# Kernel tuning notes

Hardware: AMD Instinct MI355X
Metric: run time of the kernel (lower is better)

Reference implementation:

```python
import jax, jax.numpy as jnp
import numpy as np

N_R, N_C = 20000, 5000
E_R, E_C = 320000, 80000
D_IN, HID, OUT, K = 6, 128, 3, 3
NEG_SLOPE = 0.2


def gat_layer(x, edge_index, W, a_src, a_dst, b):
    """PyG GATConv (heads=1, concat=True, add_self_loops=True), eval mode."""
    n = x.shape[0]
    loop = jnp.arange(n, dtype=edge_index.dtype)
    src = jnp.concatenate([edge_index[0], loop])
    dst = jnp.concatenate([edge_index[1], loop])
    h = x @ W                                   # [n, HID]
    e_src = h @ a_src                           # [n]
    e_dst = h @ a_dst
    e = jax.nn.leaky_relu(e_src[src] + e_dst[dst], NEG_SLOPE)  # [E+n]
    m = jax.ops.segment_max(e, dst, num_segments=n)
    m = jnp.where(jnp.isfinite(m), m, 0.0)
    ex = jnp.exp(e - m[dst])
    denom = jax.ops.segment_sum(ex, dst, num_segments=n)
    alpha = ex / jnp.maximum(denom[dst], 1e-16)
    return jax.ops.segment_sum(alpha[:, None] * h[src], dst, num_segments=n) + b


def setup_inputs() -> dict:
    key = jax.random.key(0)
    ks = jax.random.split(key, 32)
    inp = {
        "x_resting": jax.random.normal(ks[0], (N_R, D_IN), jnp.float32),
        "x_collider": jax.random.normal(ks[1], (N_C, D_IN), jnp.float32),
        "edge_index_resting": jax.random.randint(ks[2], (2, E_R), 0, N_R, jnp.int32),
        "edge_index_collider": jax.random.randint(ks[3], (2, E_C), 0, N_C, jnp.int32),
        "knn_k": K,
    }
    i = 4
    for g in ("r", "c"):
        d_in = D_IN
        for l in (1, 2):
            inp[f"W_{g}{l}"] = jax.random.normal(ks[i], (d_in, HID), jnp.float32) * (1.0 / np.sqrt(d_in)); i += 1
            inp[f"as_{g}{l}"] = jax.random.normal(ks[i], (HID,), jnp.float32) * 0.1; i += 1
            inp[f"ad_{g}{l}"] = jax.random.normal(ks[i], (HID,), jnp.float32) * 0.1; i += 1
            inp[f"b_{g}{l}"] = jnp.zeros((HID,), jnp.float32); i += 1
            d_in = HID
    inp["W_dec"] = jax.random.normal(ks[i], (2 * HID, OUT), jnp.float32) * (1.0 / np.sqrt(2 * HID)); i += 1
    inp["b_dec"] = jnp.zeros((OUT,), jnp.float32)
    return inp


def reference(x_resting, x_collider, edge_index_resting, edge_index_collider, knn_k,
              W_r1, as_r1, ad_r1, b_r1, W_r2, as_r2, ad_r2, b_r2,
              W_c1, as_c1, ad_c1, b_c1, W_c2, as_c2, ad_c2, b_c2,
              W_dec, b_dec):
    # resting branch (dropout is identity in eval mode)
    h_r = jax.nn.relu(gat_layer(x_resting, edge_index_resting, W_r1, as_r1, ad_r1, b_r1))
    h_r = jax.nn.relu(gat_layer(h_r, edge_index_resting, W_r2, as_r2, ad_r2, b_r2))
    # collider branch
    h_c = jax.nn.relu(gat_layer(x_collider, edge_index_collider, W_c1, as_c1, ad_c1, b_c1))
    h_c = jax.nn.relu(gat_layer(h_c, edge_index_collider, W_c2, as_c2, ad_c2, b_c2))
    # brute-force KNN: for each collider node, k nearest resting nodes (in feature space)
    d2 = (jnp.sum(h_c * h_c, 1)[:, None] + jnp.sum(h_r * h_r, 1)[None, :]
          - 2.0 * h_c @ h_r.T)                       # [N_C, N_R]
    _, nn_idx = jax.lax.top_k(-d2, knn_k)            # [N_C, k] indices into resting
    n_r = h_r.shape[0]
    flat_idx = nn_idx.reshape(-1)
    rep_c = jnp.repeat(h_c, knn_k, axis=0)           # x_collider[col]
    pooled_sum = jax.ops.segment_sum(rep_c, flat_idx, num_segments=n_r)
    cnt = jax.ops.segment_sum(jnp.ones((flat_idx.shape[0],), h_c.dtype), flat_idx, num_segments=n_r)
    pooled = pooled_sum / jnp.maximum(cnt, 1.0)[:, None]  # scatter_mean (0 for empty)
    x_combined = jnp.concatenate([h_r, pooled], axis=-1)
    return x_combined @ W_dec + b_dec                # new positions [N_R, 3]
```

## Files before the change

### kernel.cpp

```cpp
#include <hip/hip_runtime.h>
#include <hip/hip_bf16.h>

#define HID 128
#define NEG_SLOPE 0.2f
#define CSPLIT 8
#define KNN_CB 64
#define NCAND (CSPLIT * 12)

typedef _Float16 f16x8 __attribute__((ext_vector_type(8)));
typedef float f32x4 __attribute__((ext_vector_type(4)));

__device__ __forceinline__ bool cand_lt(float d1, int i1, float d2, int i2) {
    return d1 < d2 || (d1 == d2 && i1 < i2);
}
__device__ __forceinline__ void ins3(float s, int r, float fd[3], int fi[3]) {
    if (!cand_lt(s, r, fd[2], fi[2])) return;
    if (cand_lt(s, r, fd[0], fi[0])) {
        fd[2]=fd[1];fi[2]=fi[1]; fd[1]=fd[0];fi[1]=fi[0]; fd[0]=s;fi[0]=r;
    } else if (cand_lt(s, r, fd[1], fi[1])) {
        fd[2]=fd[1];fi[2]=fi[1]; fd[1]=s;fi[1]=r;
    } else {
        fd[2]=s;fi[2]=r;
    }
}

__global__ void k_deg(const int* __restrict__ ei, int E, int n, int* __restrict__ deg) {
    int i = blockIdx.x * blockDim.x + threadIdx.x;
    if (i >= E + n) return;
    int d = (i < E) ? ei[E + i] : i - E;
    atomicAdd(&deg[d], 1);
}

__global__ void k_chunksum(const int* __restrict__ deg, int* __restrict__ bsum, int n) {
    int t = threadIdx.x;
    int i = blockIdx.x * 256 + t;
    int v = (i < n) ? deg[i] : 0;
#pragma unroll
    for (int o = 1; o < 64; o <<= 1) v += __shfl_xor(v, o);
    __shared__ int wsum[4];
    if ((t & 63) == 0) wsum[t >> 6] = v;
    __syncthreads();
    if (t == 0) bsum[blockIdx.x] = wsum[0] + wsum[1] + wsum[2] + wsum[3];
}

__global__ void k_scan_small(int* __restrict__ a, int nb) {
    __shared__ int buf[256];
    int t = threadIdx.x;
    int v = (t < nb) ? a[t] : 0;
    buf[t] = v;
    __syncthreads();
    for (int o = 1; o < 256; o <<= 1) {
        int add = (t >= o) ? buf[t - o] : 0;
        __syncthreads();
        buf[t] += add;
        __syncthreads();
    }
    if (t < nb) a[t] = buf[t] - v;
    if (t == 0) a[nb] = buf[nb - 1];
}

__global__ void k_scan_apply(const int* __restrict__ deg, const int* __restrict__ bsum,
                             int* __restrict__ off, int* __restrict__ cur, int n) {
    __shared__ int buf[256];
    int b = blockIdx.x, t = threadIdx.x;
    int i = b * 256 + t;
    int v = (i < n) ? deg[i] : 0;
    buf[t] = v;
    __syncthreads();
    for (int o = 1; o < 256; o <<= 1) {
        int add = (t >= o) ? buf[t - o] : 0;
        __syncthreads();
        buf[t] += add;
        __syncthreads();
    }
    int excl = bsum[b] + buf[t] - v;
    if (i < n) { off[i] = excl; cur[i] = excl; }
    if (b == 0 && t == 0) off[n] = bsum[gridDim.x];
}

__global__ void k_scatter(const int* __restrict__ ei, int E, int n,
                          int* __restrict__ cursor, int* __restrict__ csr) {
    int i = blockIdx.x * blockDim.x + threadIdx.x;
    if (i >= E + n) return;
    int s, d;
    if (i < E) { s = ei[i]; d = ei[E + i]; } else { s = d = i - E; }
    int pos = atomicAdd(&cursor[d], 1);
    csr[pos] = s;
}

__global__ __launch_bounds__(128) void k_linear(
    const float* __restrict__ x, const float* __restrict__ W,
    const float* __restrict__ a_src, const float* __restrict__ a_dst,
    float* __restrict__ h, float* __restrict__ es, float* __restrict__ ed,
    int d_in, int n) {
    int n0 = blockIdx.x * 4;
    int t = threadIdx.x;
    int w = t >> 6, lane = t & 63;
    __shared__ float xs[4][HID];
    __shared__ float p1[2], p2[2];
#pragma unroll
    for (int u = 0; u < 4; ++u) {
        int node = n0 + u;
        if (t < d_in) xs[u][t] = (node < n) ? x[(size_t)node * d_in + t] : 0.f;
    }
    __syncthreads();
    float acc[4] = {0.f, 0.f, 0.f, 0.f};
    for (int k = 0; k < d_in; ++k) {
        float wv = W[k * HID + t];
#pragma unroll
        for (int u = 0; u < 4; ++u) acc[u] += xs[u][k] * wv;
    }
    float asv = a_src[t], adv = a_dst[t];
    for (int u = 0; u < 4; ++u) {
        int node = n0 + u;
        if (node >= n) break;
        h[(size_t)node * HID + t] = acc[u];
        float v1 = acc[u] * asv, v2 = acc[u] * adv;
#pragma unroll
        for (int o = 32; o > 0; o >>= 1) { v1 += __shfl_xor(v1, o); v2 += __shfl_xor(v2, o); }
        if (lane == 0) { p1[w] = v1; p2[w] = v2; }
        __syncthreads();
        if (t == 0) { es[node] = p1[0] + p1[1]; ed[node] = p2[0] + p2[1]; }
        __syncthreads();
    }
}

__global__ __launch_bounds__(256) void k_gat_csr(
    const int* __restrict__ off, const int* __restrict__ csr,
    const float* __restrict__ es, const float* __restrict__ ed,
    const float* __restrict__ h, const float* __restrict__ b,
    float* __restrict__ agg, int n,
    _Float16* __restrict__ h16, float* __restrict__ n2) {
    int node = blockIdx.x * 4 + (threadIdx.x >> 6);
    int lane = threadIdx.x & 63;
    if (node >= n) return;
    int beg = off[node], end = off[node + 1];
    float edd = ed[node];
    float m = -INFINITY;
    for (int j = beg + lane; j < end; j += 64) {
        int s = csr[j];
        float e = es[s] + edd;
        e = e > 0.f ? e : NEG_SLOPE * e;
        m = fmaxf(m, e);
    }
#pragma unroll
    for (int o = 32; o > 0; o >>= 1) m = fmaxf(m, __shfl_xor(m, o));
    float den = 0.f, a0 = 0.f, a1 = 0.f;
    int j = beg;
    for (; j + 1 < end; j += 2) {
        int s0 = csr[j], s1 = csr[j + 1];
        float e0 = es[s0] + edd;
        float e1 = es[s1] + edd;
        e0 = e0 > 0.f ? e0 : NEG_SLOPE * e0;
        e1 = e1 > 0.f ? e1 : NEG_SLOPE * e1;
        float ex0 = expf(e0 - m);
        float ex1 = expf(e1 - m);
        float h00 = h[(size_t)s0 * HID + lane];
        float h01 = h[(size_t)s0 * HID + 64 + lane];
        float h10 = h[(size_t)s1 * HID + lane];
        float h11 = h[(size_t)s1 * HID + 64 + lane];
        den += ex0 + ex1;
        a0 += ex0 * h00 + ex1 * h10;
        a1 += ex0 * h01 + ex1 * h11;
    }
    if (j < end) {
        int s0 = csr[j];
        float e0 = es[s0] + edd;
        e0 = e0 > 0.f ? e0 : NEG_SLOPE * e0;
        float ex0 = expf(e0 - m);
        den += ex0;
        a0 += ex0 * h[(size_t)s0 * HID + lane];
        a1 += ex0 * h[(size_t)s0 * HID + 64 + lane];
    }
    float inv = 1.f / fmaxf(den, 1e-16f);
    float v0 = a0 * inv + b[lane];
    float v1 = a1 * inv + b[64 + lane];
    float r0 = v0 > 0.f ? v0 : 0.f;
    float r1 = v1 > 0.f ? v1 : 0.f;
    agg[(size_t)node * HID + lane] = r0;
    agg[(size_t)node * HID + 64 + lane] = r1;
    if (h16) {
        h16[(size_t)node * HID + lane] = (_Float16)r0;
        h16[(size_t)node * HID + 64 + lane] = (_Float16)r1;
    }
    if (n2) {
        float s2 = r0 * r0 + r1 * r1;
#pragma unroll
        for (int o = 32; o > 0; o >>= 1) s2 += __shfl_xor(s2, o);
        if (lane == 0) n2[node] = s2;
    }
}

__global__ __launch_bounds__(256) void k_knn_scan(
    const _Float16* __restrict__ hr2, const _Float16* __restrict__ hc2,
    const float* __restrict__ nr2, int n_c, int n_r, int rs_chunk,
    int* __restrict__ cand_i) {
    __shared__ _Float16 lds[2][64 * HID];
    int t = threadIdx.x, w = t >> 6, lane = t & 63;
    int li = lane & 15, q = lane >> 4;
    int c0 = blockIdx.x * KNN_CB;
    int split = blockIdx.y;
    int rbeg = split * rs_chunk;
    int rows = min(rs_chunk, n_r - rbeg);
    int rend = rbeg + rows;

    if (rows <= 0) {
        int c = c0 + w * 16 + li;
        if (c < n_c) {
            size_t base = ((size_t)(c * CSPLIT + split) * 4 + q) * 3;
            for (int k = 0; k < 3; ++k) cand_i[base + k] = 0x7fffffff;
        }
        return;
    }

    f16x8 bf[4];
    {
        int c = c0 + w * 16 + li;
        int cc = min(c, n_c - 1);
#pragma unroll
        for (int ks = 0; ks < 4; ++ks)
            bf[ks] = *(const f16x8*)(hc2 + (size_t)cc * HID + ks * 32 + q * 8);
    }

    float bd[3]; int bi[3];
#pragma unroll
    for (int k = 0; k < 3; ++k) { bd[k] = INFINITY; bi[k] = 0x7fffffff; }

    int nch = (rows + 63) >> 6;

    auto STAGE = [&](int bsel, int R) {
#pragma unroll
        for (int j = 0; j < 4; ++j) {
            int row = w * 16 + j * 4 + q;
            int gr = min(R + row, n_r - 1);
            int sslot = li ^ (row & 7);
            const _Float16* src = hr2 + (size_t)gr * HID + sslot * 8;
            _Float16* dst = &lds[bsel][(w * 16 + j * 4) * HID];
            __builtin_amdgcn_global_load_lds(
                (const __attribute__((address_space(1))) void*)src,
                (__attribute__((address_space(3))) void*)dst, 16, 0, 0);
        }
    };

    STAGE(0, rbeg);
    __syncthreads();

    for (int ch = 0; ch < nch; ++ch) {
        int cur = ch & 1;
        if (ch + 1 < nch) STAGE(cur ^ 1, rbeg + (ch + 1) * 64);
        int R = rbeg + ch * 64;
        const _Float16* buf = lds[cur];
        int sw = li & 7;
        if (R + 64 <= rend) {
            float4 nrv[4];
#pragma unroll
            for (int tt = 0; tt < 4; ++tt)
                nrv[tt] = *(const float4*)(nr2 + R + tt * 16 + q * 4);
#pragma unroll
            for (int tt = 0; tt < 4; ++tt) {
                f32x4 a0 = {0.f, 0.f, 0.f, 0.f};
                int lr = tt * 16 + li;
                int swr = lr & 7;
#pragma unroll
                for (int ks = 0; ks < 4; ++ks) {
                    f16x8 af = *(const f16x8*)(&buf[lr * HID + (((ks * 4 + q) ^ swr) << 3)]);
                    a0 = __builtin_amdgcn_mfma_f32_16x16x32_f16(af, bf[ks], a0, 0, 0, 0);
                }
                int r_base = R + tt * 16 + q * 4;
                float sv[4] = {nrv[tt].x, nrv[tt].y, nrv[tt].z, nrv[tt].w};
#pragma unroll
                for (int i = 0; i < 4; ++i)
                    ins3(sv[i] - 2.f * a0[i], r_base + i, bd, bi);
            }
        } else {
            int rows_rem = rend - R;
#pragma unroll
            for (int tt = 0; tt < 4; ++tt) {
                int br = tt * 16;
                if (br < rows_rem) {
                    f32x4 a0 = {0.f, 0.f, 0.f, 0.f};
                    int lr = br + li;
                    int swr = lr & 7;
#pragma unroll
                    for (int ks = 0; ks < 4; ++ks) {
                        f16x8 af = *(const f16x8*)(&buf[lr * HID + (((ks * 4 + q) ^ swr) << 3)]);
                        a0 = __builtin_amdgcn_mfma_f32_16x16x32_f16(af, bf[ks], a0, 0, 0, 0);
                    }
                    int r_base = R + br + q * 4;
                    float4 nrv = *(const float4*)(nr2 + r_base);
                    float sv[4] = {nrv.x, nrv.y, nrv.z, nrv.w};
#pragma unroll
                    for (int i = 0; i < 4; ++i) {
                        int r = r_base + i;
                        if (r < rend) ins3(sv[i] - 2.f * a0[i], r, bd, bi);
                    }
                }
            }
        }
        (void)sw;
        __syncthreads();
    }

    {
        int c = c0 + w * 16 + li;
        if (c < n_c) {
            size_t base = ((size_t)(c * CSPLIT + split) * 4 + q) * 3;
#pragma unroll
            for (int k = 0; k < 3; ++k) cand_i[base + k] = bi[k];
        }
    }
}

__global__ __launch_bounds__(256, 4) void k_rerank(
    const int* __restrict__ cand_i, const float* __restrict__ hc,
    const float* __restrict__ hr, const float* __restrict__ nr2,
    int n_r, float* __restrict__ pooled, float* __restrict__ cnt) {
    int c = blockIdx.x;
    int t = threadIdx.x;
    __shared__ float hcs[HID];
    __shared__ int ci[NCAND];
    __shared__ float sc[NCAND];
    __shared__ int scr[NCAND];
    __shared__ int bidx[3];
    if (t < HID) hcs[t] = hc[(size_t)c * HID + t];
    if (t < NCAND) {
        int r = cand_i[(size_t)c * NCAND + t];
        ci[t] = ((unsigned)r < (unsigned)n_r) ? r : -1;
    }
    __syncthreads();

    int k4 = t & 31;
    int g = t >> 5;
    const float4* hr4 = (const float4*)hr;
    float4 a = ((const float4*)hcs)[k4];

    int rj[12];
    float4 v[12];
#pragma unroll
    for (int p = 0; p < 12; ++p) {
        rj[p] = ci[p * 8 + g];
        v[p] = hr4[(size_t)max(rj[p], 0) * 32 + k4];
    }
    float fd[3] = {INFINITY, INFINITY, INFINITY};
    int fi[3] = {0x7fffffff, 0x7fffffff, 0x7fffffff};
#pragma unroll
    for (int p = 0; p < 12; ++p) {
        float d = a.x * v[p].x + a.y * v[p].y + a.z * v[p].z + a.w * v[p].w;
#pragma unroll
        for (int o = 1; o < 32; o <<= 1) d += __shfl_xor(d, o);
        if (k4 == 0) {
            int j = p * 8 + g;
            sc[j] = (rj[p] >= 0) ? nr2[rj[p]] - 2.f * d : INFINITY;
            scr[j] = (rj[p] >= 0) ? rj[p] : 0x7fffffff;
        }
    }
    __syncthreads();
    if (t < 64) {
        ins3(sc[t], scr[t], fd, fi);
        if (t < 32) ins3(sc[64 + t], scr[64 + t], fd, fi);
#pragma unroll
        for (int o = 1; o < 64; o <<= 1) {
            float sd0 = __shfl_xor(fd[0], o), sd1 = __shfl_xor(fd[1], o), sd2 = __shfl_xor(fd[2], o);
            int si0 = __shfl_xor(fi[0], o), si1 = __shfl_xor(fi[1], o), si2 = __shfl_xor(fi[2], o);
            ins3(sd0, si0, fd, fi);
            ins3(sd1, si1, fd, fi);
            ins3(sd2, si2, fd, fi);
        }
        if (t == 0) { bidx[0] = fi[0]; bidx[1] = fi[1]; bidx[2] = fi[2]; }
    }
    __syncthreads();
    if (t < HID) {
        float hv = hcs[t];
#pragma unroll
        for (int qq = 0; qq < 3; ++qq) {
            int b = bidx[qq];
            if (b >= 0 && b < n_r) {
                atomicAdd(&pooled[(size_t)b * HID + t], hv);
                if (t == 0) atomicAdd(&cnt[b], 1.0f);
            }
        }
    }
}

__global__ void k_decode(const float* __restrict__ hr, const float* __restrict__ pooled,
                         const float* __restrict__ cnt, const float* __restrict__ Wd,
                         const float* __restrict__ bd, float* __restrict__ out, int n) {
    int node = blockIdx.x * (blockDim.x / 64) + (threadIdx.x >> 6);
    int lane = threadIdx.x & 63;
    if (node >= n) return;
    float c = fmaxf(cnt[node], 1.0f);
    float a0 = 0.f, a1 = 0.f, a2 = 0.f;
    for (int k = lane; k < HID; k += 64) {
        float v = hr[(long long)node * HID + k];
        a0 += v * Wd[k * 3 + 0];
        a1 += v * Wd[k * 3 + 1];
        a2 += v * Wd[k * 3 + 2];
        float p = pooled[(long long)node * HID + k] / c;
        a0 += p * Wd[(HID + k) * 3 + 0];
        a1 += p * Wd[(HID + k) * 3 + 1];
        a2 += p * Wd[(HID + k) * 3 + 2];
    }
    for (int off = 32; off > 0; off >>= 1) {
        a0 += __shfl_down(a0, off);
        a1 += __shfl_down(a1, off);
        a2 += __shfl_down(a2, off);
    }
    if (lane == 0) {
        out[(long long)node * 3 + 0] = a0 + bd[0];
        out[(long long)node * 3 + 1] = a1 + bd[1];
        out[(long long)node * 3 + 2] = a2 + bd[2];
    }
}

static inline int cdiv(long long a, int b) { return (int)((a + b - 1) / b); }

extern "C" void kernel_launch(void* const* d_in, const int* in_sizes, int n_in,
                              void* d_out, int out_size, void* d_ws, size_t ws_size,
                              hipStream_t stream) {
    const float* x_r = (const float*)d_in[0];
    const float* x_c = (const float*)d_in[1];
    const int* ei_r = (const int*)d_in[2];
    const int* ei_c = (const int*)d_in[3];
    const float* W_r1 = (const float*)d_in[5];
    const float* as_r1 = (const float*)d_in[6];
    const float* ad_r1 = (const float*)d_in[7];
    const float* b_r1 = (const float*)d_in[8];
    const float* W_r2 = (const float*)d_in[9];
    const float* as_r2 = (const float*)d_in[10];
    const float* ad_r2 = (const float*)d_in[11];
    const float* b_r2 = (const float*)d_in[12];
    const float* W_c1 = (const float*)d_in[13];
    const float* as_c1 = (const float*)d_in[14];
    const float* ad_c1 = (const float*)d_in[15];
    const float* b_c1 = (const float*)d_in[16];
    const float* W_c2 = (const float*)d_in[17];
    const float* as_c2 = (const float*)d_in[18];
    const float* ad_c2 = (const float*)d_in[19];
    const float* b_c2 = (const float*)d_in[20];
    const float* W_dec = (const float*)d_in[21];
    const float* b_dec = (const float*)d_in[22];
    float* out = (float*)d_out;

    const int N_R = in_sizes[0] / 6;
    const int N_C = in_sizes[1] / 6;
    const int E_R = in_sizes[2] / 2;
    const int E_C = in_sizes[3] / 2;

    float* ws = (float*)d_ws;
    size_t off = 0;
    auto alloc = [&](size_t nf) {
        float* p = ws + off;
        off += (nf + 3) & ~(size_t)3;
        return p;
    };
    float* r_h    = alloc((size_t)N_R * HID);
    float* r_agg  = alloc((size_t)N_R * HID);
    float* c_h    = alloc((size_t)N_C * HID);
    float* c_agg  = alloc((size_t)N_C * HID);
    float* pooled = alloc((size_t)N_R * HID);
    float* r_es = alloc(N_R);
    float* r_ed = alloc(N_R);
    float* c_es = alloc(N_C);
    float* c_ed = alloc(N_C);
    float* cnt = alloc(N_R);
    float* nr2 = alloc((size_t)N_R + 512);
    _Float16* hr2 = (_Float16*)alloc((size_t)N_R * HID / 2);
    _Float16* hc2 = (_Float16*)alloc((size_t)N_C * HID / 2);
    int* cand_i = (int*)alloc((size_t)N_C * NCAND);
    int* r_deg = (int*)alloc(N_R);
    int* r_off = (int*)alloc((size_t)N_R + 1);
    int* r_cur = (int*)alloc(N_R);
    int* r_csr = (int*)alloc((size_t)E_R + N_R);
    int* r_bsum = (int*)alloc(256);
    int* c_deg = (int*)alloc(N_C);
    int* c_off = (int*)alloc((size_t)N_C + 1);
    int* c_cur = (int*)alloc(N_C);
    int* c_csr = (int*)alloc((size_t)E_C + N_C);
    int* c_bsum = (int*)alloc(256);
    (void)ws_size; (void)n_in; (void)out_size;

    auto build_csr = [&](const int* ei, int E, int n, int* deg, int* offp, int* cur,
                         int* csr, int* bsum) {
        hipMemsetAsync(deg, 0, (size_t)n * sizeof(int), stream);
        k_deg<<<cdiv(E + n, 256), 256, 0, stream>>>(ei, E, n, deg);
        int nb = cdiv(n, 256);
        k_chunksum<<<nb, 256, 0, stream>>>(deg, bsum, n);
        k_scan_small<<<1, 256, 0, stream>>>(bsum, nb);
        k_scan_apply<<<nb, 256, 0, stream>>>(deg, bsum, offp, cur, n);
        k_scatter<<<cdiv(E + n, 256), 256, 0, stream>>>(ei, E, n, cur, csr);
    };
    auto gat = [&](const float* x, int d_in_dim, int n, const int* offp, const int* csr,
                   const float* W, const float* as_, const float* ad_, const float* b,
                   float* h, float* es, float* ed, float* agg,
                   _Float16* h16, float* n2) {
        k_linear<<<cdiv(n, 4), 128, 0, stream>>>(x, W, as_, ad_, h, es, ed, d_in_dim, n);
        k_gat_csr<<<cdiv(n, 4), 256, 0, stream>>>(offp, csr, es, ed, h, b, agg, n, h16, n2);
    };

    build_csr(ei_r, E_R, N_R, r_deg, r_off, r_cur, r_csr, r_bsum);
    gat(x_r, 6, N_R, r_off, r_csr, W_r1, as_r1, ad_r1, b_r1, r_h, r_es, r_ed, r_agg,
        nullptr, nullptr);
    gat(r_agg, HID, N_R, r_off, r_csr, W_r2, as_r2, ad_r2, b_r2, r_h, r_es, r_ed, r_agg,
        hr2, nr2);
    build_csr(ei_c, E_C, N_C, c_deg, c_off, c_cur, c_csr, c_bsum);
    gat(x_c, 6, N_C, c_off, c_csr, W_c1, as_c1, ad_c1, b_c1, c_h, c_es, c_ed, c_agg,
        nullptr, nullptr);
    gat(c_agg, HID, N_C, c_off, c_csr, W_c2, as_c2, ad_c2, b_c2, c_h, c_es, c_ed, c_agg,
        hc2, nullptr);

    hipMemsetAsync(pooled, 0, (size_t)N_R * HID * sizeof(float), stream);
    hipMemsetAsync(cnt, 0, (size_t)N_R * sizeof(float), stream);

    int RS = cdiv(N_R, CSPLIT * 64) * 64;
    dim3 sgrid(cdiv(N_C, KNN_CB), CSPLIT);
    k_knn_scan<<<sgrid, 256, 0, stream>>>(hr2, hc2, nr2, N_C, N_R, RS, cand_i);

    k_rerank<<<N_C, 256, 0, stream>>>(cand_i, c_agg, r_agg, nr2, N_R, pooled, cnt);

    k_decode<<<cdiv(N_R, 4), 256, 0, stream>>>(r_agg, pooled, cnt, W_dec, b_dec, out, N_R);
}
```

Baseline: 619.4 us.

## Replace atomic scatter pooling with CSR gather fused into decode

Rerank now only writes the three nearest resting indices per collider node. A histogram, scan and scatter then build a CSR from resting node to its collider neighbours, and a fused pool+decode kernel gathers and averages those features before applying the decoder. This removes the 10 MB pooled buffer memset, the float atomics into it, and the pooled read-back in decode. In exchange it adds about six small kernel launches, and the gather order can change float summation order.

```diff
diff --git a/kernel.cpp b/kernel.cpp
--- a/kernel.cpp
+++ b/kernel.cpp
@@ -86,6 +86,24 @@
     if (i < E) { s = ei[i]; d = ei[E + i]; } else { s = d = i - E; }
     int pos = atomicAdd(&cursor[d], 1);
     csr[pos] = s;
+}
+
+__global__ void k_nn_hist(const int* __restrict__ nn, int m, int n_r, int* __restrict__ cnt) {
+    int i = blockIdx.x * blockDim.x + threadIdx.x;
+    if (i >= m) return;
+    int r = nn[i];
+    if ((unsigned)r < (unsigned)n_r) atomicAdd(&cnt[r], 1);
+}
+
+__global__ void k_nn_scatter(const int* __restrict__ nn, int m, int n_r,
+                             int* __restrict__ cur, int* __restrict__ plist) {
+    int i = blockIdx.x * blockDim.x + threadIdx.x;
+    if (i >= m) return;
+    int r = nn[i];
+    if ((unsigned)r < (unsigned)n_r) {
+        int pos = atomicAdd(&cur[r], 1);
+        plist[pos] = i / 3;
+    }
 }
 
 __global__ __launch_bounds__(128) void k_linear(
@@ -250,7 +268,6 @@
         if (ch + 1 < nch) STAGE(cur ^ 1, rbeg + (ch + 1) * 64);
         int R = rbeg + ch * 64;
         const _Float16* buf = lds[cur];
-        int sw = li & 7;
         if (R + 64 <= rend) {
             float4 nrv[4];
 #pragma unroll
@@ -297,7 +314,6 @@
                 }
             }
         }
-        (void)sw;
         __syncthreads();
     }
 
@@ -314,14 +330,13 @@
 __global__ __launch_bounds__(256, 4) void k_rerank(
     const int* __restrict__ cand_i, const float* __restrict__ hc,
     const float* __restrict__ hr, const float* __restrict__ nr2,
-    int n_r, float* __restrict__ pooled, float* __restrict__ cnt) {
+    int n_r, int* __restrict__ nn_idx) {
     int c = blockIdx.x;
     int t = threadIdx.x;
     __shared__ float hcs[HID];
     __shared__ int ci[NCAND];
     __shared__ float sc[NCAND];
     __shared__ int scr[NCAND];
-    __shared__ int bidx[3];
     if (t < HID) hcs[t] = hc[(size_t)c * HID + t];
     if (t < NCAND) {
         int r = cand_i[(size_t)c * NCAND + t];
@@ -366,49 +381,50 @@
             ins3(sd1, si1, fd, fi);
             ins3(sd2, si2, fd, fi);
         }
-        if (t == 0) { bidx[0] = fi[0]; bidx[1] = fi[1]; bidx[2] = fi[2]; }
-    }
-    __syncthreads();
-    if (t < HID) {
-        float hv = hcs[t];
-#pragma unroll
-        for (int qq = 0; qq < 3; ++qq) {
-            int b = bidx[qq];
-            if (b >= 0 && b < n_r) {
-                atomicAdd(&pooled[(size_t)b * HID + t], hv);
-                if (t == 0) atomicAdd(&cnt[b], 1.0f);
-            }
-        }
-    }
-}
-
-__global__ void k_decode(const float* __restrict__ hr, const float* __restrict__ pooled,
-                         const float* __restrict__ cnt, const float* __restrict__ Wd,
-                         const float* __restrict__ bd, float* __restrict__ out, int n) {
-    int node = blockIdx.x * (blockDim.x / 64) + (threadIdx.x >> 6);
+        if (t == 0) {
+            nn_idx[c * 3 + 0] = fi[0];
+            nn_idx[c * 3 + 1] = fi[1];
+            nn_idx[c * 3 + 2] = fi[2];
+        }
+    }
+}
+
+__global__ __launch_bounds__(256) void k_pool_decode(
+    const int* __restrict__ poff, const int* __restrict__ plist,
+    const float* __restrict__ hc, const float* __restrict__ hr,
+    const float* __restrict__ Wd, const float* __restrict__ bd,
+    float* __restrict__ out, int n) {
+    int node = blockIdx.x * 4 + (threadIdx.x >> 6);
     int lane = threadIdx.x & 63;
     if (node >= n) return;
-    float c = fmaxf(cnt[node], 1.0f);
-    float a0 = 0.f, a1 = 0.f, a2 = 0.f;
-    for (int k = lane; k < HID; k += 64) {
-        float v = hr[(long long)node * HID + k];
-        a0 += v * Wd[k * 3 + 0];
-        a1 += v * Wd[k * 3 + 1];
-        a2 += v * Wd[k * 3 + 2];
-        float p = pooled[(long long)node * HID + k] / c;
-        a0 += p * Wd[(HID + k) * 3 + 0];
-        a1 += p * Wd[(HID + k) * 3 + 1];
-        a2 += p * Wd[(HID + k) * 3 + 2];
-    }
-    for (int off = 32; off > 0; off >>= 1) {
-        a0 += __shfl_down(a0, off);
-        a1 += __shfl_down(a1, off);
-        a2 += __shfl_down(a2, off);
+    int beg = poff[node], end = poff[node + 1];
+    float p0 = 0.f, p1 = 0.f;
+    for (int j = beg; j < end; ++j) {
+        int c = plist[j];
+        p0 += hc[(size_t)c * HID + lane];
+        p1 += hc[(size_t)c * HID + 64 + lane];
+    }
+    float inv = 1.f / fmaxf((float)(end - beg), 1.f);
+    p0 *= inv;
+    p1 *= inv;
+    float h0 = hr[(size_t)node * HID + lane];
+    float h1 = hr[(size_t)node * HID + 64 + lane];
+    float a0 = h0 * Wd[lane * 3 + 0] + h1 * Wd[(64 + lane) * 3 + 0]
+             + p0 * Wd[(HID + lane) * 3 + 0] + p1 * Wd[(HID + 64 + lane) * 3 + 0];
+    float a1 = h0 * Wd[lane * 3 + 1] + h1 * Wd[(64 + lane) * 3 + 1]
+             + p0 * Wd[(HID + lane) * 3 + 1] + p1 * Wd[(HID + 64 + lane) * 3 + 1];
+    float a2 = h0 * Wd[lane * 3 + 2] + h1 * Wd[(64 + lane) * 3 + 2]
+             + p0 * Wd[(HID + lane) * 3 + 2] + p1 * Wd[(HID + 64 + lane) * 3 + 2];
+#pragma unroll
+    for (int o = 32; o > 0; o >>= 1) {
+        a0 += __shfl_xor(a0, o);
+        a1 += __shfl_xor(a1, o);
+        a2 += __shfl_xor(a2, o);
     }
     if (lane == 0) {
-        out[(long long)node * 3 + 0] = a0 + bd[0];
-        out[(long long)node * 3 + 1] = a1 + bd[1];
-        out[(long long)node * 3 + 2] = a2 + bd[2];
+        out[(size_t)node * 3 + 0] = a0 + bd[0];
+        out[(size_t)node * 3 + 1] = a1 + bd[1];
+        out[(size_t)node * 3 + 2] = a2 + bd[2];
     }
 }
 
@@ -457,16 +473,15 @@
     float* r_agg  = alloc((size_t)N_R * HID);
     float* c_h    = alloc((size_t)N_C * HID);
     float* c_agg  = alloc((size_t)N_C * HID);
-    float* pooled = alloc((size_t)N_R * HID);
     float* r_es = alloc(N_R);
     float* r_ed = alloc(N_R);
     float* c_es = alloc(N_C);
     float* c_ed = alloc(N_C);
-    float* cnt = alloc(N_R);
     float* nr2 = alloc((size_t)N_R + 512);
     _Float16* hr2 = (_Float16*)alloc((size_t)N_R * HID / 2);
     _Float16* hc2 = (_Float16*)alloc((size_t)N_C * HID / 2);
     int* cand_i = (int*)alloc((size_t)N_C * NCAND);
+    int* nn_idx = (int*)alloc((size_t)N_C * 3);
     int* r_deg = (int*)alloc(N_R);
     int* r_off = (int*)alloc((size_t)N_R + 1);
     int* r_cur = (int*)alloc(N_R);
@@ -477,6 +492,11 @@
     int* c_cur = (int*)alloc(N_C);
     int* c_csr = (int*)alloc((size_t)E_C + N_C);
     int* c_bsum = (int*)alloc(256);
+    int* p_cnt = (int*)alloc(N_R);
+    int* p_off = (int*)alloc((size_t)N_R + 1);
+    int* p_cur = (int*)alloc(N_R);
+    int* p_list = (int*)alloc((size_t)N_C * 3);
+    int* p_bsum = (int*)alloc(256);
     (void)ws_size; (void)n_in; (void)out_size;
 
     auto build_csr = [&](const int* ei, int E, int n, int* deg, int* offp, int* cur,
@@ -508,14 +528,23 @@
     gat(c_agg, HID, N_C, c_off, c_csr, W_c2, as_c2, ad_c2, b_c2, c_h, c_es, c_ed, c_agg,
         hc2, nullptr);
 
-    hipMemsetAsync(pooled, 0, (size_t)N_R * HID * sizeof(float), stream);
-    hipMemsetAsync(cnt, 0, (size_t)N_R * sizeof(float), stream);
-
     int RS = cdiv(N_R, CSPLIT * 64) * 64;
     dim3 sgrid(cdiv(N_C, KNN_CB), CSPLIT);
     k_knn_scan<<<sgrid, 256, 0, stream>>>(hr2, hc2, nr2, N_C, N_R, RS, cand_i);
 
-    k_rerank<<<N_C, 256, 0, stream>>>(cand_i, c_agg, r_agg, nr2, N_R, pooled, cnt);
-
-    k_decode<<<cdiv(N_R, 4), 256, 0, stream>>>(r_agg, pooled, cnt, W_dec, b_dec, out, N_R);
-}
+    k_rerank<<<N_C, 256, 0, stream>>>(cand_i, c_agg, r_agg, nr2, N_R, nn_idx);
+
+    {
+        int m = N_C * 3;
+        hipMemsetAsync(p_cnt, 0, (size_t)N_R * sizeof(int), stream);
+        k_nn_hist<<<cdiv(m, 256), 256, 0, stream>>>(nn_idx, m, N_R, p_cnt);
+        int nb = cdiv(N_R, 256);
+        k_chunksum<<<nb, 256, 0, stream>>>(p_cnt, p_bsum, N_R);
+        k_scan_small<<<1, 256, 0, stream>>>(p_bsum, nb);
+        k_scan_apply<<<nb, 256, 0, stream>>>(p_cnt, p_bsum, p_off, p_cur, N_R);
+        k_nn_scatter<<<cdiv(m, 256), 256, 0, stream>>>(nn_idx, m, N_R, p_cur, p_list);
+    }
+
+    k_pool_decode<<<cdiv(N_R, 4), 256, 0, stream>>>(p_off, p_list, c_agg, r_agg,
+                                                    W_dec, b_dec, out, N_R);
+}
```

After: 1.786 ms. +188.4%, slower.
